# Kernel optimization log

Hardware: AMD Instinct MI355X
Metric: run time of the kernel (lower is better)

The kernel has to match this reference:

```python
import jax, jax.numpy as jnp
import numpy as np

N_NODES = 100000
NEG_SLOPE = 0.01  # F.leaky_relu default


def _gin_mean_layer(x, src, dst):
    """DGL GINConv(aggregator='mean', apply_func=None, eps=0, activation=leaky_relu).
    out = leaky_relu((1+eps)*x + mean_{in-neighbors} x_src), nodes with no in-edges get mean=0.
    """
    msg_sum = jax.ops.segment_sum(x[src], dst, num_segments=N_NODES)  # [N, D]
    deg = jax.ops.segment_sum(jnp.ones(src.shape, dtype=x.dtype), dst, num_segments=N_NODES)  # [N]
    mean = msg_sum / jnp.maximum(deg, 1.0)[:, None]
    return jax.nn.leaky_relu(x + mean, negative_slope=NEG_SLOPE)


def setup_inputs() -> dict:
    key = jax.random.key(0)
    k0, k1, k2, k3, k4 = jax.random.split(key, 5)
    n_edges = 640000
    d = 128
    return {
        "node_features": jax.random.normal(k0, (N_NODES, d), dtype=jnp.float32),
        "edges1_src": jax.random.randint(k1, (n_edges,), 0, N_NODES, dtype=jnp.int64),
        "edges1_dst": jax.random.randint(k2, (n_edges,), 0, N_NODES, dtype=jnp.int64),
        "edges2_src": jax.random.randint(k3, (n_edges,), 0, N_NODES, dtype=jnp.int64),
        "edges2_dst": jax.random.randint(k4, (n_edges,), 0, N_NODES, dtype=jnp.int64),
    }


def reference(node_features, edges1_src, edges1_dst, edges2_src, edges2_dst):
    h_AC1 = _gin_mean_layer(node_features, edges1_src, edges1_dst)
    h_CA1 = _gin_mean_layer(node_features, edges2_src, edges2_dst)
    h = jnp.concatenate((h_AC1, h_CA1), axis=1)  # [N, 2D]
    h_AC2 = _gin_mean_layer(h, edges1_src, edges1_dst)
    h_CA2 = _gin_mean_layer(h, edges2_src, edges2_dst)
    return jnp.concatenate((h_AC2, h_CA2), axis=1)  # [N, 4D]
```

## Files before the change

kernel.cpp:

```cpp
#include <hip/hip_runtime.h>

#define N_NODES 100000
#define NEG 0.01f
#define CAP 32

typedef float f4v __attribute__((ext_vector_type(4)));

__device__ __forceinline__ float lrelu(float v) { return v > 0.f ? v : NEG * v; }

__device__ __forceinline__ unsigned int f2bf(float f) {
    unsigned int x = __float_as_uint(f);
    return (x + 0x7fffu + ((x >> 16) & 1u)) >> 16;
}
__device__ __forceinline__ unsigned int pack2bf(float lo, float hi) {
    return f2bf(lo) | (f2bf(hi) << 16);
}
__device__ __forceinline__ float bf_lo(unsigned int u) { return __uint_as_float(u << 16); }
__device__ __forceinline__ float bf_hi(unsigned int u) { return __uint_as_float(u & 0xffff0000u); }

__device__ __forceinline__ void unpack8(uint4 u, float* f) {
    f[0] = bf_lo(u.x); f[1] = bf_hi(u.x);
    f[2] = bf_lo(u.y); f[3] = bf_hi(u.y);
    f[4] = bf_lo(u.z); f[5] = bf_hi(u.z);
    f[6] = bf_lo(u.w); f[7] = bf_hi(u.w);
}

__global__ void build_both(const int* __restrict__ s1, const int* __restrict__ d1a, int E1,
                           const int* __restrict__ s2, const int* __restrict__ d2a, int E2,
                           int* __restrict__ deg1, int* __restrict__ slots1,
                           int* __restrict__ deg2, int* __restrict__ slots2) {
    int i = blockIdx.x * blockDim.x + threadIdx.x;
    if (i < E1) {
        int d = d1a[i];
        int pos = atomicAdd(&deg1[d], 1);
        if (pos < CAP) slots1[d * CAP + pos] = s1[i];
    }
    int k = i - E1;
    if (k >= 0 && k < E2) {
        int d = d2a[k];
        int pos = atomicAdd(&deg2[d], 1);
        if (pos < CAP) slots2[d * CAP + pos] = s2[k];
    }
}

__global__ void convert_x(const float4* __restrict__ x, uint4* __restrict__ xb) {
    int i = blockIdx.x * blockDim.x + threadIdx.x;
    if (i >= N_NODES * 16) return;
    float4 v0 = x[2 * i];
    float4 v1 = x[2 * i + 1];
    uint4 p;
    p.x = pack2bf(v0.x, v0.y);
    p.y = pack2bf(v0.z, v0.w);
    p.z = pack2bf(v1.x, v1.y);
    p.w = pack2bf(v1.z, v1.w);
    xb[i] = p;
}

__global__ void __launch_bounds__(256) layer1(
        const uint4* __restrict__ x4,
        const int* __restrict__ deg1, const int* __restrict__ slots1,
        const int* __restrict__ deg2, const int* __restrict__ slots2,
        uint4* __restrict__ h4) {
    int gid = blockIdx.x * blockDim.x + threadIdx.x;
    int n = gid >> 6;
    if (n >= N_NODES) return;
    int lane = gid & 63;
    int t = lane & 15;
    int g = lane >> 4;

    uint4 xv = x4[(size_t)n * 16 + t];

    int d1 = deg1[n], d2 = deg2[n];
    int m1 = min(d1, CAP), m2 = min(d2, CAP);
    int my1 = (lane < m1) ? slots1[n * CAP + lane] : 0;
    int my2 = (lane < m2) ? slots2[n * CAP + lane] : 0;

    float a[8] = {0.f, 0.f, 0.f, 0.f, 0.f, 0.f, 0.f, 0.f};
    float b[8] = {0.f, 0.f, 0.f, 0.f, 0.f, 0.f, 0.f, 0.f};

    for (int j0 = 0; j0 < m1; j0 += 4) {
        int j = j0 + g;
        int s = __shfl(my1, j);
        uint4 u = make_uint4(0u, 0u, 0u, 0u);
        if (j < m1) u = x4[(size_t)s * 16 + t];
        float f[8]; unpack8(u, f);
        #pragma unroll
        for (int i = 0; i < 8; ++i) a[i] += f[i];
    }
    for (int j0 = 0; j0 < m2; j0 += 4) {
        int j = j0 + g;
        int s = __shfl(my2, j);
        uint4 u = make_uint4(0u, 0u, 0u, 0u);
        if (j < m2) u = x4[(size_t)s * 16 + t];
        float f[8]; unpack8(u, f);
        #pragma unroll
        for (int i = 0; i < 8; ++i) b[i] += f[i];
    }

    #pragma unroll
    for (int i = 0; i < 8; ++i) {
        a[i] += __shfl_xor(a[i], 16);
        a[i] += __shfl_xor(a[i], 32);
        b[i] += __shfl_xor(b[i], 16);
        b[i] += __shfl_xor(b[i], 32);
    }

    float xf[8]; unpack8(xv, xf);
    float r1 = 1.f / (float)max(d1, 1);
    float r2 = 1.f / (float)max(d2, 1);

    if (g == 0) {
        uint4 o;
        o.x = pack2bf(lrelu(xf[0] + a[0] * r1), lrelu(xf[1] + a[1] * r1));
        o.y = pack2bf(lrelu(xf[2] + a[2] * r1), lrelu(xf[3] + a[3] * r1));
        o.z = pack2bf(lrelu(xf[4] + a[4] * r1), lrelu(xf[5] + a[5] * r1));
        o.w = pack2bf(lrelu(xf[6] + a[6] * r1), lrelu(xf[7] + a[7] * r1));
        h4[(size_t)n * 32 + t] = o;
    } else if (g == 1) {
        uint4 o;
        o.x = pack2bf(lrelu(xf[0] + b[0] * r2), lrelu(xf[1] + b[1] * r2));
        o.y = pack2bf(lrelu(xf[2] + b[2] * r2), lrelu(xf[3] + b[3] * r2));
        o.z = pack2bf(lrelu(xf[4] + b[4] * r2), lrelu(xf[5] + b[5] * r2));
        o.w = pack2bf(lrelu(xf[6] + b[6] * r2), lrelu(xf[7] + b[7] * r2));
        h4[(size_t)n * 32 + 16 + t] = o;
    }
}

__global__ void __launch_bounds__(256) layer2(
        const uint4* __restrict__ h4,
        const int* __restrict__ deg1, const int* __restrict__ slots1,
        const int* __restrict__ deg2, const int* __restrict__ slots2,
        float4* __restrict__ out4) {
    int gid = blockIdx.x * blockDim.x + threadIdx.x;
    int n = gid >> 6;
    if (n >= N_NODES) return;
    int lane = gid & 63;
    int t = lane & 31;
    int g = lane >> 5;

    uint4 hv = h4[(size_t)n * 32 + t];

    int d1 = deg1[n], d2 = deg2[n];
    int m1 = min(d1, CAP), m2 = min(d2, CAP);
    int my1 = (lane < m1) ? slots1[n * CAP + lane] : 0;
    int my2 = (lane < m2) ? slots2[n * CAP + lane] : 0;

    float a[8] = {0.f, 0.f, 0.f, 0.f, 0.f, 0.f, 0.f, 0.f};
    float b[8] = {0.f, 0.f, 0.f, 0.f, 0.f, 0.f, 0.f, 0.f};

    for (int j0 = 0; j0 < m1; j0 += 2) {
        int j = j0 + g;
        int s = __shfl(my1, j);
        uint4 u = make_uint4(0u, 0u, 0u, 0u);
        if (j < m1) u = h4[(size_t)s * 32 + t];
        float f[8]; unpack8(u, f);
        #pragma unroll
        for (int i = 0; i < 8; ++i) a[i] += f[i];
    }
    for (int j0 = 0; j0 < m2; j0 += 2) {
        int j = j0 + g;
        int s = __shfl(my2, j);
        uint4 u = make_uint4(0u, 0u, 0u, 0u);
        if (j < m2) u = h4[(size_t)s * 32 + t];
        float f[8]; unpack8(u, f);
        #pragma unroll
        for (int i = 0; i < 8; ++i) b[i] += f[i];
    }

    #pragma unroll
    for (int i = 0; i < 8; ++i) {
        a[i] += __shfl_xor(a[i], 32);
        b[i] += __shfl_xor(b[i], 32);
    }

    float hf[8]; unpack8(hv, hf);
    float r1 = 1.f / (float)max(d1, 1);
    float r2 = 1.f / (float)max(d2, 1);

    f4v* ob = (f4v*)out4;
    if (g == 0) {
        f4v A0 = {lrelu(hf[0] + a[0] * r1), lrelu(hf[1] + a[1] * r1),
                  lrelu(hf[2] + a[2] * r1), lrelu(hf[3] + a[3] * r1)};
        f4v A1 = {lrelu(hf[4] + a[4] * r1), lrelu(hf[5] + a[5] * r1),
                  lrelu(hf[6] + a[6] * r1), lrelu(hf[7] + a[7] * r1)};
        __builtin_nontemporal_store(A0, &ob[(size_t)n * 128 + 2 * t]);
        __builtin_nontemporal_store(A1, &ob[(size_t)n * 128 + 2 * t + 1]);
    } else {
        f4v B0 = {lrelu(hf[0] + b[0] * r2), lrelu(hf[1] + b[1] * r2),
                  lrelu(hf[2] + b[2] * r2), lrelu(hf[3] + b[3] * r2)};
        f4v B1 = {lrelu(hf[4] + b[4] * r2), lrelu(hf[5] + b[5] * r2),
                  lrelu(hf[6] + b[6] * r2), lrelu(hf[7] + b[7] * r2)};
        __builtin_nontemporal_store(B0, &ob[(size_t)n * 128 + 64 + 2 * t]);
        __builtin_nontemporal_store(B1, &ob[(size_t)n * 128 + 64 + 2 * t + 1]);
    }
}

extern "C" void kernel_launch(void* const* d_in, const int* in_sizes, int n_in,
                              void* d_out, int out_size, void* d_ws, size_t ws_size,
                              hipStream_t stream) {
    const float* x = (const float*)d_in[0];
    const int* e1s = (const int*)d_in[1];
    const int* e1d = (const int*)d_in[2];
    const int* e2s = (const int*)d_in[3];
    const int* e2d = (const int*)d_in[4];
    const int E1 = in_sizes[1];
    const int E2 = in_sizes[3];
    float* out = (float*)d_out;

    int* deg1   = (int*)d_ws;
    int* deg2   = deg1 + N_NODES;
    int* slots1 = deg2 + N_NODES;
    int* slots2 = slots1 + (size_t)N_NODES * CAP;
    unsigned int* xb = (unsigned int*)(slots2 + (size_t)N_NODES * CAP);
    unsigned int* hb = xb + (size_t)N_NODES * 64;

    hipMemsetAsync(deg1, 0, 2ull * N_NODES * sizeof(int), stream);

    build_both<<<(E1 + E2 + 255) / 256, 256, 0, stream>>>(
        e1s, e1d, E1, e2s, e2d, E2, deg1, slots1, deg2, slots2);
    convert_x<<<(N_NODES * 16 + 255) / 256, 256, 0, stream>>>(
        (const float4*)x, (uint4*)xb);

    int blocks = (N_NODES + 3) / 4;
    layer1<<<blocks, 256, 0, stream>>>(
        (const uint4*)xb, deg1, slots1, deg2, slots2, (uint4*)hb);
    layer2<<<blocks, 256, 0, stream>>>(
        (const uint4*)hb, deg1, slots1, deg2, slots2, (float4*)out);
}
```

Baseline: 520.2 us.

## Merge edge-list loops with prefetch and fuse build with convert kernel

Fuses the CSR-slot build and the bf16 conversion into one launch with block-range dispatch, removing a kernel launch and letting both run concurrently. In both layer kernels, the two separate neighbour gather loops become one loop over the concatenated slot lists, with software prefetch of the next gathered row and predicated accumulation into the two sums. This shortens the serial loop tail and hides gather latency, at the cost of extra selects per element and an extra live register vector.

```diff
diff --git a/kernel.cpp b/kernel.cpp
--- a/kernel.cpp
+++ b/kernel.cpp
@@ -25,35 +25,38 @@
     f[6] = bf_lo(u.w); f[7] = bf_hi(u.w);
 }
 
-__global__ void build_both(const int* __restrict__ s1, const int* __restrict__ d1a, int E1,
-                           const int* __restrict__ s2, const int* __restrict__ d2a, int E2,
-                           int* __restrict__ deg1, int* __restrict__ slots1,
-                           int* __restrict__ deg2, int* __restrict__ slots2) {
-    int i = blockIdx.x * blockDim.x + threadIdx.x;
-    if (i < E1) {
-        int d = d1a[i];
-        int pos = atomicAdd(&deg1[d], 1);
-        if (pos < CAP) slots1[d * CAP + pos] = s1[i];
-    }
-    int k = i - E1;
-    if (k >= 0 && k < E2) {
-        int d = d2a[k];
-        int pos = atomicAdd(&deg2[d], 1);
-        if (pos < CAP) slots2[d * CAP + pos] = s2[k];
-    }
-}
-
-__global__ void convert_x(const float4* __restrict__ x, uint4* __restrict__ xb) {
-    int i = blockIdx.x * blockDim.x + threadIdx.x;
-    if (i >= N_NODES * 16) return;
-    float4 v0 = x[2 * i];
-    float4 v1 = x[2 * i + 1];
-    uint4 p;
-    p.x = pack2bf(v0.x, v0.y);
-    p.y = pack2bf(v0.z, v0.w);
-    p.z = pack2bf(v1.x, v1.y);
-    p.w = pack2bf(v1.z, v1.w);
-    xb[i] = p;
+__global__ void __launch_bounds__(256) build_and_convert(
+        const int* __restrict__ s1, const int* __restrict__ d1a, int E1,
+        const int* __restrict__ s2, const int* __restrict__ d2a, int E2,
+        int* __restrict__ deg1, int* __restrict__ slots1,
+        int* __restrict__ deg2, int* __restrict__ slots2,
+        const float4* __restrict__ x, uint4* __restrict__ xb, int convBlocks) {
+    int b = blockIdx.x;
+    if (b < convBlocks) {
+        int i = b * 256 + threadIdx.x;
+        if (i >= N_NODES * 16) return;
+        float4 v0 = x[2 * i];
+        float4 v1 = x[2 * i + 1];
+        uint4 p;
+        p.x = pack2bf(v0.x, v0.y);
+        p.y = pack2bf(v0.z, v0.w);
+        p.z = pack2bf(v1.x, v1.y);
+        p.w = pack2bf(v1.z, v1.w);
+        xb[i] = p;
+    } else {
+        int i = (b - convBlocks) * 256 + threadIdx.x;
+        if (i < E1) {
+            int d = d1a[i];
+            int pos = atomicAdd(&deg1[d], 1);
+            if (pos < CAP) slots1[d * CAP + pos] = s1[i];
+        }
+        int k = i - E1;
+        if (k >= 0 && k < E2) {
+            int d = d2a[k];
+            int pos = atomicAdd(&deg2[d], 1);
+            if (pos < CAP) slots2[d * CAP + pos] = s2[k];
+        }
+    }
 }
 
 __global__ void __launch_bounds__(256) layer1(
@@ -72,29 +75,32 @@
 
     int d1 = deg1[n], d2 = deg2[n];
     int m1 = min(d1, CAP), m2 = min(d2, CAP);
-    int my1 = (lane < m1) ? slots1[n * CAP + lane] : 0;
-    int my2 = (lane < m2) ? slots2[n * CAP + lane] : 0;
+    int M = m1 + m2;
+
+    int idx = 0;
+    if (lane < m1) idx = slots1[n * CAP + lane];
+    else if (lane - m1 < m2) idx = slots2[n * CAP + (lane - m1)];
 
     float a[8] = {0.f, 0.f, 0.f, 0.f, 0.f, 0.f, 0.f, 0.f};
     float b[8] = {0.f, 0.f, 0.f, 0.f, 0.f, 0.f, 0.f, 0.f};
 
-    for (int j0 = 0; j0 < m1; j0 += 4) {
-        int j = j0 + g;
-        int s = __shfl(my1, j);
-        uint4 u = make_uint4(0u, 0u, 0u, 0u);
-        if (j < m1) u = x4[(size_t)s * 16 + t];
-        float f[8]; unpack8(u, f);
+    int s0 = __shfl(idx, g);
+    uint4 u = make_uint4(0u, 0u, 0u, 0u);
+    if (g < M) u = x4[(size_t)s0 * 16 + t];
+    for (int j0 = 0; j0 < M; j0 += 4) {
+        uint4 cur = u;
+        int jc = j0 + g;
+        bool isA = jc < m1;
+        int jn = jc + 4;
+        int sn = __shfl(idx, jn & 63);
+        u = make_uint4(0u, 0u, 0u, 0u);
+        if (jn < M) u = x4[(size_t)sn * 16 + t];
+        float f[8]; unpack8(cur, f);
         #pragma unroll
-        for (int i = 0; i < 8; ++i) a[i] += f[i];
-    }
-    for (int j0 = 0; j0 < m2; j0 += 4) {
-        int j = j0 + g;
-        int s = __shfl(my2, j);
-        uint4 u = make_uint4(0u, 0u, 0u, 0u);
-        if (j < m2) u = x4[(size_t)s * 16 + t];
-        float f[8]; unpack8(u, f);
-        #pragma unroll
-        for (int i = 0; i < 8; ++i) b[i] += f[i];
+        for (int i = 0; i < 8; ++i) {
+            a[i] += isA ? f[i] : 0.f;
+            b[i] += isA ? 0.f : f[i];
+        }
     }
 
     #pragma unroll
@@ -142,29 +148,32 @@
 
     int d1 = deg1[n], d2 = deg2[n];
     int m1 = min(d1, CAP), m2 = min(d2, CAP);
-    int my1 = (lane < m1) ? slots1[n * CAP + lane] : 0;
-    int my2 = (lane < m2) ? slots2[n * CAP + lane] : 0;
+    int M = m1 + m2;
+
+    int idx = 0;
+    if (lane < m1) idx = slots1[n * CAP + lane];
+    else if (lane - m1 < m2) idx = slots2[n * CAP + (lane - m1)];
 
     float a[8] = {0.f, 0.f, 0.f, 0.f, 0.f, 0.f, 0.f, 0.f};
     float b[8] = {0.f, 0.f, 0.f, 0.f, 0.f, 0.f, 0.f, 0.f};
 
-    for (int j0 = 0; j0 < m1; j0 += 2) {
-        int j = j0 + g;
-        int s = __shfl(my1, j);
-        uint4 u = make_uint4(0u, 0u, 0u, 0u);
-        if (j < m1) u = h4[(size_t)s * 32 + t];
-        float f[8]; unpack8(u, f);
+    int s0 = __shfl(idx, g);
+    uint4 u = make_uint4(0u, 0u, 0u, 0u);
+    if (g < M) u = h4[(size_t)s0 * 32 + t];
+    for (int j0 = 0; j0 < M; j0 += 2) {
+        uint4 cur = u;
+        int jc = j0 + g;
+        bool isA = jc < m1;
+        int jn = jc + 2;
+        int sn = __shfl(idx, jn & 63);
+        u = make_uint4(0u, 0u, 0u, 0u);
+        if (jn < M) u = h4[(size_t)sn * 32 + t];
+        float f[8]; unpack8(cur, f);
         #pragma unroll
-        for (int i = 0; i < 8; ++i) a[i] += f[i];
-    }
-    for (int j0 = 0; j0 < m2; j0 += 2) {
-        int j = j0 + g;
-        int s = __shfl(my2, j);
-        uint4 u = make_uint4(0u, 0u, 0u, 0u);
-        if (j < m2) u = h4[(size_t)s * 32 + t];
-        float f[8]; unpack8(u, f);
-        #pragma unroll
-        for (int i = 0; i < 8; ++i) b[i] += f[i];
+        for (int i = 0; i < 8; ++i) {
+            a[i] += isA ? f[i] : 0.f;
+            b[i] += isA ? 0.f : f[i];
+        }
     }
 
     #pragma unroll
@@ -216,10 +225,11 @@
 
     hipMemsetAsync(deg1, 0, 2ull * N_NODES * sizeof(int), stream);
 
-    build_both<<<(E1 + E2 + 255) / 256, 256, 0, stream>>>(
-        e1s, e1d, E1, e2s, e2d, E2, deg1, slots1, deg2, slots2);
-    convert_x<<<(N_NODES * 16 + 255) / 256, 256, 0, stream>>>(
-        (const float4*)x, (uint4*)xb);
+    int convBlocks = (N_NODES * 16 + 255) / 256;
+    int edgeBlocks = (E1 + E2 + 255) / 256;
+    build_and_convert<<<convBlocks + edgeBlocks, 256, 0, stream>>>(
+        e1s, e1d, E1, e2s, e2d, E2, deg1, slots1, deg2, slots2,
+        (const float4*)x, (uint4*)xb, convBlocks);
 
     int blocks = (N_NODES + 3) / 4;
     layer1<<<blocks, 256, 0, stream>>>(
```

Measured after the change: 521.7 us. About the same (+0.3%).
